# Performance work log

Hardware: AMD Instinct MI355X
Metric: run time of the kernel (lower is better)

## Reference

```python
import jax, jax.numpy as jnp
import numpy as np

B, S, D = 2, 1024, 1024
E, K, F, FS = 8, 2, 512, 1024

def setup_inputs() -> dict:
    key = jax.random.key(0)
    ks = jax.random.split(key, 9)
    s = lambda k, shape, fan: jax.random.normal(k, shape, jnp.float32) * (fan ** -0.5)
    return {
        "x": jax.random.normal(ks[0], (B, S, D), jnp.float32),
        "Wr": s(ks[1], (D, E), D),
        "Wg": s(ks[2], (E, D, F), D),
        "Wu": s(ks[3], (E, D, F), D),
        "Wd": s(ks[4], (E, F, D), F),
        "Sg": s(ks[5], (D, FS), D),
        "Su": s(ks[6], (D, FS), D),
        "Sd": s(ks[7], (FS, D), FS),
        "expert_bias": jnp.zeros((E,), jnp.float32),
    }

def reference(x, Wr, Wg, Wu, Wd, Sg, Su, Sd, expert_bias):
    b, s, d = x.shape
    xf = x.reshape(-1, d)                              # [T, D]
    T = xf.shape[0]
    logits = xf @ Wr + expert_bias                     # [T, E]
    top_v, top_i = jax.lax.top_k(logits, K)            # [T, K]
    probs = jax.nn.softmax(top_v, axis=-1)             # [T, K]
    # dense routing-weight matrix: zero for non-selected experts
    rw = jnp.zeros_like(logits).at[jnp.arange(T)[:, None], top_i].set(probs)  # [T, E]
    # SwiGLU experts, computed densely; routing weight zeros out unselected
    gate = jnp.einsum('td,edf->tef', xf, Wg)           # [T, E, F]
    up = jnp.einsum('td,edf->tef', xf, Wu)
    h = jax.nn.silu(gate) * up
    eo = jnp.einsum('tef,efd->ted', h, Wd)             # [T, E, D]
    out = jnp.einsum('te,ted->td', rw, eo)             # [T, D]
    # shared expert applied to all tokens
    out = out + (jax.nn.silu(xf @ Sg) * (xf @ Su)) @ Sd
    return out.reshape(b, s, d)
```

## Files before the change

### kernel.cpp

```cpp
#include <hip/hip_runtime.h>
#include <cstdint>
#include <cstddef>

typedef __attribute__((ext_vector_type(8))) short bf16x8;
typedef __attribute__((ext_vector_type(4))) float f32x4;

#define AS1 __attribute__((address_space(1)))
#define AS3 __attribute__((address_space(3)))

__device__ __forceinline__ unsigned short f2bf(float f) {
  union { float f; unsigned int u; } v; v.f = f;
  unsigned int r = v.u + 0x7fffu + ((v.u >> 16) & 1u);
  return (unsigned short)(r >> 16);
}

__device__ __forceinline__ void gll16(const unsigned short* g, unsigned short* l) {
  __builtin_amdgcn_global_load_lds((const AS1 void*)g, (AS3 void*)l, 16, 0, 0);
}


__global__ __launch_bounds__(256) void transpose_cvt_all(
    const float* __restrict__ Wg, const float* __restrict__ Wu,
    const float* __restrict__ Wd, const float* __restrict__ Sg,
    const float* __restrict__ Su, const float* __restrict__ Sd,
    const float* __restrict__ x, const float* __restrict__ Wr,
    unsigned short* __restrict__ WguT, unsigned short* __restrict__ WdT,
    unsigned short* __restrict__ SguT, unsigned short* __restrict__ SdT,
    unsigned short* __restrict__ Xb, float* __restrict__ logits) {
  const int z = blockIdx.z;
  const int tid = threadIdx.x;

  if (z == 31) {
    const int bid = blockIdx.y * 16 + blockIdx.x;
    const int wave = tid >> 6;
    const int lane = tid & 63;
#pragma unroll
    for (int it = 0; it < 2; it++) {
      const int t = bid * 8 + wave * 2 + it;
      const float* xr = x + (size_t)t * 1024;
      float acc[8];
#pragma unroll
      for (int e = 0; e < 8; e++) acc[e] = 0.f;
#pragma unroll
      for (int i = 0; i < 16; i++) {
        int d = lane + i * 64;
        float xv = xr[d];
        const float4* w = (const float4*)(Wr + d * 8);
        float4 w0 = w[0], w1 = w[1];
        acc[0] += xv * w0.x; acc[1] += xv * w0.y; acc[2] += xv * w0.z; acc[3] += xv * w0.w;
        acc[4] += xv * w1.x; acc[5] += xv * w1.y; acc[6] += xv * w1.z; acc[7] += xv * w1.w;
      }
#pragma unroll
      for (int off = 32; off > 0; off >>= 1)
#pragma unroll
        for (int e = 0; e < 8; e++) acc[e] += __shfl_down(acc[e], off);
      if (lane == 0) {
#pragma unroll
        for (int e = 0; e < 8; e++) logits[t * 8 + e] = acc[e];
      }
    }
    return;
  }

  if (z >= 27) {
    size_t off = (size_t)(z - 27) * 524288 + blockIdx.y * 32768 + blockIdx.x * 2048 + tid * 8;
    const float4* s = (const float4*)(x + off);
    float4 a = s[0], b = s[1];
    bf16x8 o = { (short)f2bf(a.x), (short)f2bf(a.y), (short)f2bf(a.z), (short)f2bf(a.w),
                 (short)f2bf(b.x), (short)f2bf(b.y), (short)f2bf(b.z), (short)f2bf(b.w) };
    *(bf16x8*)(Xb + off) = o;
    return;
  }

  const float* src; unsigned short* base; int R, C, nmul, nadd, Ksz;
  if (z < 8)       { src = Wg + (size_t)z * 524288; base = WguT + (size_t)z * 1048576; R = 1024; C = 512;  nmul = 2; nadd = 0; Ksz = 1024; }
  else if (z < 16) { src = Wu + (size_t)(z - 8) * 524288; base = WguT + (size_t)(z - 8) * 1048576; R = 1024; C = 512; nmul = 2; nadd = 1; Ksz = 1024; }
  else if (z < 24) { src = Wd + (size_t)(z - 16) * 524288; base = WdT + (size_t)(z - 16) * 524288; R = 512; C = 1024; nmul = 1; nadd = 0; Ksz = 512; }
  else if (z == 24){ src = Sg; base = SguT; R = 1024; C = 1024; nmul = 2; nadd = 0; Ksz = 1024; }
  else if (z == 25){ src = Su; base = SguT; R = 1024; C = 1024; nmul = 2; nadd = 1; Ksz = 1024; }
  else             { src = Sd; base = SdT; R = 1024; C = 1024; nmul = 1; nadd = 0; Ksz = 1024; }
  const int c0 = blockIdx.x * 64, r0 = blockIdx.y * 64;
  if (c0 >= C || r0 >= R) return;

  __shared__ float tile[64][65];
  {
    const int row = tid >> 2, cs = (tid & 3) * 16;
    const float* sp = src + (size_t)(r0 + row) * C + c0 + cs;
#pragma unroll
    for (int k = 0; k < 4; k++) {
      float4 v = ((const float4*)sp)[k];
      tile[row][cs + k * 4 + 0] = v.x; tile[row][cs + k * 4 + 1] = v.y;
      tile[row][cs + k * 4 + 2] = v.z; tile[row][cs + k * 4 + 3] = v.w;
    }
  }
  __syncthreads();
#pragma unroll
  for (int i = 0; i < 2; i++) {
    const int cc = i * 32 + (tid >> 3);
    const int rseg = (tid & 7) * 8;
    bf16x8 o;
#pragma unroll
    for (int j = 0; j < 8; j++) o[j] = (short)f2bf(tile[rseg + j][cc]);
    const int n = nmul * (c0 + cc) + nadd;
    const int k0 = r0 + rseg;
    const int p = n >> 7, r = n & 127, s = k0 >> 5;
    const int c4 = ((k0 >> 3) & 3) ^ ((r >> 1) & 3);
    *(bf16x8*)(base + (size_t)p * (Ksz * 128) + (size_t)s * 4096 + (r * 4 + c4) * 8) = o;
  }
}

__global__ __launch_bounds__(1024) void assign_kernel(
    const float* __restrict__ logits, const float* __restrict__ bias,
    int* __restrict__ list, int* __restrict__ ridx, float* __restrict__ rp,
    int* __restrict__ counts_g, int* __restrict__ offs_g) {
  __shared__ int cnt[8];
  __shared__ int offs[9];
  const int tid = threadIdx.x;
  if (tid < 8) cnt[tid] = 0;
  __syncthreads();
  int te[2][2], tpos[2][2];
  float tp[2][2];
#pragma unroll
  for (int it = 0; it < 2; it++) {
    int t = tid + it * 1024;
    float v[8];
#pragma unroll
    for (int e = 0; e < 8; e++) v[e] = logits[t * 8 + e] + bias[e];
    int i0 = 0;
#pragma unroll
    for (int e = 1; e < 8; e++) if (v[e] > v[i0]) i0 = e;
    int i1 = (i0 == 0) ? 1 : 0;
#pragma unroll
    for (int e = 0; e < 8; e++) if (e != i0 && v[e] > v[i1]) i1 = e;
    float pa = 1.f / (1.f + __expf(v[i1] - v[i0]));
    te[it][0] = i0; te[it][1] = i1;
    tp[it][0] = pa; tp[it][1] = 1.f - pa;
    tpos[it][0] = atomicAdd(&cnt[i0], 1);
    tpos[it][1] = atomicAdd(&cnt[i1], 1);
  }
  __syncthreads();
  if (tid == 0) {
    int s = 0;
#pragma unroll
    for (int e = 0; e < 8; e++) { offs[e] = s; s += cnt[e]; }
    offs[8] = s;
#pragma unroll
    for (int e = 0; e < 8; e++) { counts_g[e] = cnt[e]; offs_g[e] = offs[e]; }
    offs_g[8] = s;
  }
  __syncthreads();
#pragma unroll
  for (int it = 0; it < 2; it++) {
    int t = tid + it * 1024;
#pragma unroll
    for (int k = 0; k < 2; k++) {
      int grow = offs[te[it][k]] + tpos[it][k];
      list[grow] = t;
      ridx[t * 2 + k] = grow;
      rp[t * 2 + k] = tp[it][k];
    }
  }
}

#define STAGE4(buf, s) { \
  unsigned short* Ad = As + (buf) * 4096 + wuni2; \
  unsigned short* Bd = Bs + (buf) * 4096 + wuni2; \
  gll16(gA0 + (s) * 32, Ad); \
  gll16(gA1 + (s) * 32, Ad + 512); \
  gll16(gB + (s) * 4096, Bd); \
  gll16(gB + (s) * 4096 + 512, Bd + 512); }

template <int NK>
__device__ __forceinline__ void kloop32(
    const unsigned short* gA0, const unsigned short* gA1,
    const unsigned short* gB,
    unsigned short* As, unsigned short* Bs, const int wuni2,
    const int aO0, const int aO1, const int aO2, const int aO3,
    const int bO0, const int bO1, const int bO2, const int bO3,
    f32x4 (&acc)[4][4]) {
  STAGE4(0, 0);
  STAGE4(1, 1);
#pragma unroll
  for (int i = 0; i < NK; ++i) {
    if (i + 1 < NK) asm volatile("s_waitcnt vmcnt(4) lgkmcnt(0)\n\ts_barrier" ::: "memory");
    else            asm volatile("s_waitcnt vmcnt(0) lgkmcnt(0)\n\ts_barrier" ::: "memory");
    if (i + 2 < NK) { STAGE4((i + 2) % 3, i + 2); }
    const unsigned short* Ab = As + (i % 3) * 4096;
    const unsigned short* Bb = Bs + (i % 3) * 4096;
    bf16x8 af[4], bf[4];
    af[0] = *(const bf16x8*)(Ab + aO0);
    af[1] = *(const bf16x8*)(Ab + aO1);
    af[2] = *(const bf16x8*)(Ab + aO2);
    af[3] = *(const bf16x8*)(Ab + aO3);
    bf[0] = *(const bf16x8*)(Bb + bO0);
    bf[1] = *(const bf16x8*)(Bb + bO1);
    bf[2] = *(const bf16x8*)(Bb + bO2);
    bf[3] = *(const bf16x8*)(Bb + bO3);
    __builtin_amdgcn_s_setprio(1);
#pragma unroll
    for (int ii = 0; ii < 4; ++ii)
#pragma unroll
      for (int jj = 0; jj < 4; ++jj)
        acc[ii][jj] = __builtin_amdgcn_mfma_f32_16x16x32_bf16(af[ii], bf[jj], acc[ii][jj], 0, 0, 0);
    __builtin_amdgcn_s_setprio(0);
  }
}

template <int MODE>
__global__ __launch_bounds__(256, 3) void gemm_tn_kernel(
    const unsigned short* __restrict__ Xb, const unsigned short* __restrict__ He,
    const unsigned short* __restrict__ Hs, const unsigned short* __restrict__ Wgu,
    const unsigned short* __restrict__ Sgu, const unsigned short* __restrict__ Wd,
    const unsigned short* __restrict__ Sd, unsigned short* __restrict__ HeOut,
    unsigned short* __restrict__ HsOut, float* __restrict__ De, float* __restrict__ Ds,
    const int* __restrict__ list, const int* __restrict__ counts,
    const int* __restrict__ offs) {
  const int h = blockIdx.x;
  const int c = h & 7;
  const int idx = h >> 3;

  int cnt, lda, m0, n0;
  bool routed;
  const unsigned short* A;
  const unsigned short* Bt;
  const int* alist = nullptr;
  unsigned short* H = nullptr;
  float* D = nullptr;
  int ldh = 0;

  if (MODE == 0) {
    if (idx < 128) {
      routed = true;
      n0 = (idx >> 4) * 128; m0 = (idx & 15) * 128;
      cnt = counts[c]; A = Xb; alist = list + offs[c]; lda = 1024;
      Bt = Wgu + (size_t)c * 1048576 + (size_t)(n0 >> 7) * 131072;
      H = HeOut + (size_t)offs[c] * 512; ldh = 512;
    } else {
      routed = false;
      const int t2 = idx - 128;
      m0 = ((c & 1) * 8 + (t2 & 7)) * 128;
      n0 = ((c >> 1) * 4 + (t2 >> 3)) * 128;
      cnt = 2048; A = Xb; lda = 1024;
      Bt = Sgu + (size_t)(n0 >> 7) * 131072;
      H = HsOut; ldh = 1024;
    }
  } else {
    if (idx < 128) {
      routed = true;
      n0 = (idx >> 4) * 128; m0 = (idx & 15) * 128;
      cnt = counts[c]; A = He + (size_t)offs[c] * 512; lda = 512;
      Bt = Wd + (size_t)c * 524288 + (size_t)(n0 >> 7) * 65536;
      D = De + (size_t)offs[c] * 1024;
    } else {
      routed = false;
      const int t2 = idx - 128;
      m0 = ((c & 1) * 8 + (t2 & 7)) * 128;
      n0 = ((c >> 1) * 2 + (t2 >> 3)) * 128;
      cnt = 2048; A = Hs; lda = 1024;
      Bt = Sd + (size_t)(n0 >> 7) * 131072;
      D = Ds;
    }
  }
  if (m0 >= cnt) return;

  __shared__ unsigned short As[3 * 4096];
  __shared__ unsigned short Bs[3 * 4096];

  const int tid = threadIdx.x;
  const int wave = tid >> 6;
  const int lane = tid & 63;
  const int wuni2 = wave * 1024;

  const int achk = ((lane & 3) ^ ((lane >> 3) & 3)) * 8;
  const int arow0 = wave * 32 + (lane >> 2);
  const int arow1 = arow0 + 16;

  int r0 = m0 + arow0; if (r0 >= cnt) r0 = cnt - 1;
  int r1 = m0 + arow1; if (r1 >= cnt) r1 = cnt - 1;
  size_t ab0, ab1;
  if (MODE == 0 && routed) {
    ab0 = (size_t)alist[r0] * lda; ab1 = (size_t)alist[r1] * lda;
  } else {
    ab0 = (size_t)r0 * lda; ab1 = (size_t)r1 * lda;
  }
  const unsigned short* gA0 = A + ab0 + achk;
  const unsigned short* gA1 = A + ab1 + achk;
  const unsigned short* gB = Bt + (wave * 128 + lane) * 8;

  const int wm = (wave & 1) * 64;
  const int wn = (wave >> 1) * 64;
  const int fl = lane & 15;
  const int q = lane >> 4;

  const int cr = (q ^ ((fl >> 1) & 3)) * 8;
  const int aO0 = (wm + fl) * 32 + cr, aO1 = aO0 + 512, aO2 = aO0 + 1024, aO3 = aO0 + 1536;
  const int bO0 = (wn + fl) * 32 + cr, bO1 = bO0 + 512, bO2 = bO0 + 1024, bO3 = bO0 + 1536;

  f32x4 acc[4][4];
  f32x4 zero = {0.f, 0.f, 0.f, 0.f};
#pragma unroll
  for (int i = 0; i < 4; i++)
#pragma unroll
    for (int j = 0; j < 4; j++) acc[i][j] = zero;

  if (MODE == 1 && routed)
    kloop32<16>(gA0, gA1, gB, As, Bs, wuni2, aO0, aO1, aO2, aO3, bO0, bO1, bO2, bO3, acc);
  else
    kloop32<32>(gA0, gA1, gB, As, Bs, wuni2, aO0, aO1, aO2, aO3, bO0, bO1, bO2, bO3, acc);

  if (MODE == 0) {
#pragma unroll
    for (int i = 0; i < 4; i++) {
#pragma unroll
      for (int j = 0; j < 4; j++) {
#pragma unroll
        for (int r = 0; r < 4; r++) {
          int grow = m0 + wm + i * 16 + q * 4 + r;
          float v = acc[i][j][r];
          float pv = __shfl_xor(v, 1);
          if ((lane & 1) == 0 && grow < cnt) {
            float s = v / (1.f + __expf(-v));
            int colh = (n0 + wn + j * 16 + fl) >> 1;
            H[(size_t)grow * ldh + colh] = f2bf(s * pv);
          }
        }
      }
    }
  } else {
#pragma unroll
    for (int i = 0; i < 4; i++) {
#pragma unroll
      for (int r = 0; r < 4; r++) {
        int grow = m0 + wm + i * 16 + q * 4 + r;
        if (grow >= cnt) continue;
#pragma unroll
        for (int j = 0; j < 4; j++) {
          int col = n0 + wn + j * 16 + fl;
          D[(size_t)grow * 1024 + col] = acc[i][j][r];
        }
      }
    }
  }
}

__global__ __launch_bounds__(256) void combine_kernel(
    const float* __restrict__ Ds, const float* __restrict__ De,
    const int* __restrict__ ridx, const float* __restrict__ rp,
    float* __restrict__ out) {
  const int t = blockIdx.x;
  const int i0 = ridx[t * 2], i1 = ridx[t * 2 + 1];
  const float p0 = rp[t * 2], p1 = rp[t * 2 + 1];
  const float4* a  = (const float4*)(Ds + (size_t)t * 1024);
  const float4* b0 = (const float4*)(De + (size_t)i0 * 1024);
  const float4* b1 = (const float4*)(De + (size_t)i1 * 1024);
  float4* o = (float4*)(out + (size_t)t * 1024);
  int c = threadIdx.x;
  float4 va = a[c], v0 = b0[c], v1 = b1[c];
  float4 r;
  r.x = va.x + p0 * v0.x + p1 * v1.x;
  r.y = va.y + p0 * v0.y + p1 * v1.y;
  r.z = va.z + p0 * v0.z + p1 * v1.z;
  r.w = va.w + p0 * v0.w + p1 * v1.w;
  o[c] = r;
}

extern "C" void kernel_launch(void* const* d_in, const int* in_sizes, int n_in,
                              void* d_out, int out_size, void* d_ws, size_t ws_size,
                              hipStream_t stream) {
  const float* x    = (const float*)d_in[0];
  const float* Wr   = (const float*)d_in[1];
  const float* Wg   = (const float*)d_in[2];
  const float* Wu   = (const float*)d_in[3];
  const float* Wd   = (const float*)d_in[4];
  const float* Sg   = (const float*)d_in[5];
  const float* Su   = (const float*)d_in[6];
  const float* Sd   = (const float*)d_in[7];
  const float* bias = (const float*)d_in[8];
  float* out = (float*)d_out;

  char* ws = (char*)d_ws;
  size_t o = 0;
  auto alloc = [&](size_t b) { char* p = ws + o; o += (b + 255) & ~(size_t)255; return p; };
  unsigned short* Xb   = (unsigned short*)alloc((size_t)2048 * 1024 * 2);
  unsigned short* WguT = (unsigned short*)alloc((size_t)8 * 1024 * 1024 * 2);
  unsigned short* WdT  = (unsigned short*)alloc((size_t)8 * 1024 * 512 * 2);
  unsigned short* SguT = (unsigned short*)alloc((size_t)2048 * 1024 * 2);
  unsigned short* SdT  = (unsigned short*)alloc((size_t)1024 * 1024 * 2);
  float* logits = (float*)alloc((size_t)2048 * 8 * 4);
  int*   list   = (int*)alloc((size_t)4096 * 4);
  int*   ridx   = (int*)alloc((size_t)2048 * 2 * 4);
  float* rp     = (float*)alloc((size_t)2048 * 2 * 4);
  int*   counts = (int*)alloc(64);
  int*   offs   = (int*)alloc(64);
  unsigned short* He = (unsigned short*)alloc((size_t)4096 * 512 * 2);
  unsigned short* Hs = (unsigned short*)alloc((size_t)2048 * 1024 * 2);
  float* De = (float*)alloc((size_t)4096 * 1024 * 4);
  float* Ds = (float*)alloc((size_t)2048 * 1024 * 4);

  transpose_cvt_all<<<dim3(16, 16, 32), 256, 0, stream>>>(Wg, Wu, Wd, Sg, Su, Sd, x, Wr,
                                                          WguT, WdT, SguT, SdT, Xb, logits);

  assign_kernel<<<1, 1024, 0, stream>>>(logits, bias, list, ridx, rp, counts, offs);

  gemm_tn_kernel<0><<<dim3(1280), 256, 0, stream>>>(
      Xb, He, Hs, WguT, SguT, WdT, SdT, He, Hs, De, Ds, list, counts, offs);
  gemm_tn_kernel<1><<<dim3(1152), 256, 0, stream>>>(
      Xb, He, Hs, WguT, SguT, WdT, SdT, He, Hs, De, Ds, list, counts, offs);

  combine_kernel<<<2048, 256, 0, stream>>>(Ds, De, ridx, rp, out);
}
```

Measured before the change: 195.5 us.

## Fuse combine into down-proj GEMM epilogue via atomics; deepen LDS pipeline to 4 stages

Removes the combine kernel and the De/Ds fp32 intermediates. The down-projection GEMM epilogue now atomically adds the routing-weighted results straight into the output, which is zeroed by an extra slice of the preprocessing kernel. The GEMM k-loop also moves from triple to quad buffering with prefetch distance 3, and occupancy drops to 2 blocks per CU to fit the larger LDS footprint. The trade is atomic contention and non-deterministic summation order, plus fewer resident blocks, in exchange for less global traffic and one fewer launch.

```diff
diff --git a/kernel.cpp b/kernel.cpp
--- a/kernel.cpp
+++ b/kernel.cpp
@@ -26,9 +26,19 @@
     const float* __restrict__ x, const float* __restrict__ Wr,
     unsigned short* __restrict__ WguT, unsigned short* __restrict__ WdT,
     unsigned short* __restrict__ SguT, unsigned short* __restrict__ SdT,
-    unsigned short* __restrict__ Xb, float* __restrict__ logits) {
+    unsigned short* __restrict__ Xb, float* __restrict__ logits,
+    float* __restrict__ out) {
   const int z = blockIdx.z;
   const int tid = threadIdx.x;
+
+  if (z == 32) {
+    const int bid = blockIdx.y * 16 + blockIdx.x;
+    float4* o = (float4*)out;
+    float4 zz = {0.f, 0.f, 0.f, 0.f};
+#pragma unroll
+    for (int it = 0; it < 8; it++) o[bid * 2048 + it * 256 + tid] = zz;
+    return;
+  }
 
   if (z == 31) {
     const int bid = blockIdx.y * 16 + blockIdx.x;
@@ -111,7 +121,7 @@
 
 __global__ __launch_bounds__(1024) void assign_kernel(
     const float* __restrict__ logits, const float* __restrict__ bias,
-    int* __restrict__ list, int* __restrict__ ridx, float* __restrict__ rp,
+    int* __restrict__ list, float* __restrict__ ps,
     int* __restrict__ counts_g, int* __restrict__ offs_g) {
   __shared__ int cnt[8];
   __shared__ int offs[9];
@@ -156,8 +166,7 @@
     for (int k = 0; k < 2; k++) {
       int grow = offs[te[it][k]] + tpos[it][k];
       list[grow] = t;
-      ridx[t * 2 + k] = grow;
-      rp[t * 2 + k] = tp[it][k];
+      ps[grow] = tp[it][k];
     }
   }
 }
@@ -180,13 +189,15 @@
     f32x4 (&acc)[4][4]) {
   STAGE4(0, 0);
   STAGE4(1, 1);
+  STAGE4(2, 2);
 #pragma unroll
   for (int i = 0; i < NK; ++i) {
-    if (i + 1 < NK) asm volatile("s_waitcnt vmcnt(4) lgkmcnt(0)\n\ts_barrier" ::: "memory");
-    else            asm volatile("s_waitcnt vmcnt(0) lgkmcnt(0)\n\ts_barrier" ::: "memory");
-    if (i + 2 < NK) { STAGE4((i + 2) % 3, i + 2); }
-    const unsigned short* Ab = As + (i % 3) * 4096;
-    const unsigned short* Bb = Bs + (i % 3) * 4096;
+    if (i + 2 < NK)      asm volatile("s_waitcnt vmcnt(8) lgkmcnt(0)\n\ts_barrier" ::: "memory");
+    else if (i + 1 < NK) asm volatile("s_waitcnt vmcnt(4) lgkmcnt(0)\n\ts_barrier" ::: "memory");
+    else                 asm volatile("s_waitcnt vmcnt(0) lgkmcnt(0)\n\ts_barrier" ::: "memory");
+    if (i + 3 < NK) { STAGE4((i + 3) & 3, i + 3); }
+    const unsigned short* Ab = As + (i & 3) * 4096;
+    const unsigned short* Bb = Bs + (i & 3) * 4096;
     bf16x8 af[4], bf[4];
     af[0] = *(const bf16x8*)(Ab + aO0);
     af[1] = *(const bf16x8*)(Ab + aO1);
@@ -207,25 +218,24 @@
 }
 
 template <int MODE>
-__global__ __launch_bounds__(256, 3) void gemm_tn_kernel(
+__global__ __launch_bounds__(256, 2) void gemm_tn_kernel(
     const unsigned short* __restrict__ Xb, const unsigned short* __restrict__ He,
     const unsigned short* __restrict__ Hs, const unsigned short* __restrict__ Wgu,
     const unsigned short* __restrict__ Sgu, const unsigned short* __restrict__ Wd,
     const unsigned short* __restrict__ Sd, unsigned short* __restrict__ HeOut,
-    unsigned short* __restrict__ HsOut, float* __restrict__ De, float* __restrict__ Ds,
-    const int* __restrict__ list, const int* __restrict__ counts,
-    const int* __restrict__ offs) {
+    unsigned short* __restrict__ HsOut, float* __restrict__ out,
+    const int* __restrict__ list, const float* __restrict__ ps,
+    const int* __restrict__ counts, const int* __restrict__ offs) {
   const int h = blockIdx.x;
   const int c = h & 7;
   const int idx = h >> 3;
 
-  int cnt, lda, m0, n0;
+  int cnt, lda, m0, n0, gbase = 0;
   bool routed;
   const unsigned short* A;
   const unsigned short* Bt;
   const int* alist = nullptr;
   unsigned short* H = nullptr;
-  float* D = nullptr;
   int ldh = 0;
 
   if (MODE == 0) {
@@ -248,9 +258,9 @@
     if (idx < 128) {
       routed = true;
       n0 = (idx >> 4) * 128; m0 = (idx & 15) * 128;
-      cnt = counts[c]; A = He + (size_t)offs[c] * 512; lda = 512;
+      gbase = offs[c];
+      cnt = counts[c]; A = He + (size_t)gbase * 512; lda = 512;
       Bt = Wd + (size_t)c * 524288 + (size_t)(n0 >> 7) * 65536;
-      D = De + (size_t)offs[c] * 1024;
     } else {
       routed = false;
       const int t2 = idx - 128;
@@ -258,13 +268,12 @@
       n0 = ((c >> 1) * 2 + (t2 >> 3)) * 128;
       cnt = 2048; A = Hs; lda = 1024;
       Bt = Sd + (size_t)(n0 >> 7) * 131072;
-      D = Ds;
     }
   }
   if (m0 >= cnt) return;
 
-  __shared__ unsigned short As[3 * 4096];
-  __shared__ unsigned short Bs[3 * 4096];
+  __shared__ unsigned short As[4 * 4096];
+  __shared__ unsigned short Bs[4 * 4096];
 
   const int tid = threadIdx.x;
   const int wave = tid >> 6;
@@ -333,35 +342,18 @@
       for (int r = 0; r < 4; r++) {
         int grow = m0 + wm + i * 16 + q * 4 + r;
         if (grow >= cnt) continue;
+        int t; float p;
+        if (routed) { int g = gbase + grow; t = list[g]; p = ps[g]; }
+        else        { t = grow; p = 1.f; }
+        float* orow = out + (size_t)t * 1024;
 #pragma unroll
         for (int j = 0; j < 4; j++) {
           int col = n0 + wn + j * 16 + fl;
-          D[(size_t)grow * 1024 + col] = acc[i][j][r];
+          unsafeAtomicAdd(orow + col, p * acc[i][j][r]);
         }
       }
     }
   }
-}
-
-__global__ __launch_bounds__(256) void combine_kernel(
-    const float* __restrict__ Ds, const float* __restrict__ De,
-    const int* __restrict__ ridx, const float* __restrict__ rp,
-    float* __restrict__ out) {
-  const int t = blockIdx.x;
-  const int i0 = ridx[t * 2], i1 = ridx[t * 2 + 1];
-  const float p0 = rp[t * 2], p1 = rp[t * 2 + 1];
-  const float4* a  = (const float4*)(Ds + (size_t)t * 1024);
-  const float4* b0 = (const float4*)(De + (size_t)i0 * 1024);
-  const float4* b1 = (const float4*)(De + (size_t)i1 * 1024);
-  float4* o = (float4*)(out + (size_t)t * 1024);
-  int c = threadIdx.x;
-  float4 va = a[c], v0 = b0[c], v1 = b1[c];
-  float4 r;
-  r.x = va.x + p0 * v0.x + p1 * v1.x;
-  r.y = va.y + p0 * v0.y + p1 * v1.y;
-  r.z = va.z + p0 * v0.z + p1 * v1.z;
-  r.w = va.w + p0 * v0.w + p1 * v1.w;
-  o[c] = r;
 }
 
 extern "C" void kernel_launch(void* const* d_in, const int* in_sizes, int n_in,
@@ -388,24 +380,19 @@
   unsigned short* SdT  = (unsigned short*)alloc((size_t)1024 * 1024 * 2);
   float* logits = (float*)alloc((size_t)2048 * 8 * 4);
   int*   list   = (int*)alloc((size_t)4096 * 4);
-  int*   ridx   = (int*)alloc((size_t)2048 * 2 * 4);
-  float* rp     = (float*)alloc((size_t)2048 * 2 * 4);
+  float* ps     = (float*)alloc((size_t)4096 * 4);
   int*   counts = (int*)alloc(64);
   int*   offs   = (int*)alloc(64);
   unsigned short* He = (unsigned short*)alloc((size_t)4096 * 512 * 2);
   unsigned short* Hs = (unsigned short*)alloc((size_t)2048 * 1024 * 2);
-  float* De = (float*)alloc((size_t)4096 * 1024 * 4);
-  float* Ds = (float*)alloc((size_t)2048 * 1024 * 4);
-
-  transpose_cvt_all<<<dim3(16, 16, 32), 256, 0, stream>>>(Wg, Wu, Wd, Sg, Su, Sd, x, Wr,
-                                                          WguT, WdT, SguT, SdT, Xb, logits);
-
-  assign_kernel<<<1, 1024, 0, stream>>>(logits, bias, list, ridx, rp, counts, offs);
+
+  transpose_cvt_all<<<dim3(16, 16, 33), 256, 0, stream>>>(Wg, Wu, Wd, Sg, Su, Sd, x, Wr,
+                                                          WguT, WdT, SguT, SdT, Xb, logits, out);
+
+  assign_kernel<<<1, 1024, 0, stream>>>(logits, bias, list, ps, counts, offs);
 
   gemm_tn_kernel<0><<<dim3(1280), 256, 0, stream>>>(
-      Xb, He, Hs, WguT, SguT, WdT, SdT, He, Hs, De, Ds, list, counts, offs);
+      Xb, He, Hs, WguT, SguT, WdT, SdT, He, Hs, out, list, ps, counts, offs);
   gemm_tn_kernel<1><<<dim3(1152), 256, 0, stream>>>(
-      Xb, He, Hs, WguT, SguT, WdT, SdT, He, Hs, De, Ds, list, counts, offs);
-
-  combine_kernel<<<2048, 256, 0, stream>>>(Ds, De, ridx, rp, out);
-}
+      Xb, He, Hs, WguT, SguT, WdT, SdT, He, Hs, out, list, ps, counts, offs);
+}
```

New measurement: 225.7 us. +15.5%, slower.
